# Kernel tuning notes

Measured on AMD Instinct MI355X. Metric: run time of the kernel, lower is better.

Reference implementation:

```python
import jax, jax.numpy as jnp
import numpy as np
from jax.scipy.special import logsumexp

N, K, D = 131072, 256, 32


def setup_inputs() -> dict:
    key = jax.random.key(0)
    k1, k2, k3 = jax.random.split(key, 3)
    points = jax.random.normal(k1, (N, D), dtype=jnp.float32)
    centers = jax.random.uniform(k2, (K, D), dtype=jnp.float32)
    # well-conditioned inverse-sqrt covariances (original used 15*I; scaled to
    # avoid float32 overflow in sqrt(det(covs_inv)) for D=32)
    covs_inv_sqrt = (0.5 * jnp.broadcast_to(jnp.eye(D, dtype=jnp.float32), (K, D, D))
                     + 0.02 * jax.random.normal(k3, (K, D, D), dtype=jnp.float32))
    weights = jnp.ones((K,), dtype=jnp.float32)
    threshold = jnp.zeros((1,), dtype=jnp.float32)
    return {"points": points, "centers": centers,
            "covs_inv_sqrt": covs_inv_sqrt, "weights": weights,
            "threshold": threshold}


def reference(points, centers, covs_inv_sqrt, weights, threshold):
    # refresh(): equal_clusters=True branch
    w = jnp.abs(weights)
    center_prs = w / (w.sum() + 1e-30)                       # [K]
    covs_inv = jnp.einsum('kde,kfe->kdf', covs_inv_sqrt, covs_inv_sqrt)  # [K,D,D]
    coefs = center_prs * jnp.sqrt(jnp.linalg.det(covs_inv))  # [K]

    # pairwise weighted sqdist: q_ij = (x_i - c_j)^T A_j (x_i - c_j)
    B = covs_inv.reshape(K, D * D)                           # [K, D*D]
    X2 = (points[:, :, None] * points[:, None, :]).reshape(N, D * D)  # [N, D*D]
    t_xAx = X2 @ B.T                                         # [N, K]
    m = jnp.einsum('kde,ke->kd', covs_inv, centers)          # A_j c_j, [K,D]
    t_xAc = points @ m.T                                     # [N, K]
    t_cAc = jnp.einsum('kd,kd->k', m, centers)               # [K]
    d_ij = -0.5 * (t_xAx - 2.0 * t_xAc + t_cAc[None, :])     # [N, K]

    # weighted logsumexp over centers, then subtract threshold
    ll = logsumexp(d_ij, axis=1, b=coefs[None, :])           # [N]
    return ll[:, None] - threshold[0]                        # [N, 1]
```

## Files before the change

kernel.cpp:

```cpp
#include <hip/hip_runtime.h>
#include <math.h>

#define NPTS 131072
#define KCOMP 256
#define DIM 32
#define KF 608
#define PSIF_BYTES 311296
#define WS_NEED (PSIF_BYTES + KCOMP * 4)

typedef __attribute__((ext_vector_type(8))) short short8;
typedef __attribute__((ext_vector_type(16))) float f32x16;

__device__ __forceinline__ unsigned short f2bf(float v) {
    unsigned u = __float_as_uint(v);
    u += 0x7fffu + ((u >> 16) & 1u);
    return (unsigned short)(u >> 16);
}

constexpr int L4c(int d) { return ((32 - d + 3) / 4) * 4; }
constexpr int PfxC(int d) { int s = 0; for (int i = 0; i < d; ++i) s += L4c(i); return s; }
constexpr int rowOfC(int p) { int d = 0; while (d < 31 && PfxC(d + 1) <= p) ++d; return d; }
constexpr int dOfC(int p) { return (p >= 576) ? -1 : rowOfC(p); }
constexpr int f0OfC(int p) {
    return (p >= 576) ? (p - 576) : ((rowOfC(p) & ~3) + (p - PfxC(rowOfC(p))));
}

__global__ __launch_bounds__(256) void gmm_pre(
    const float* __restrict__ S,
    const float* __restrict__ centers,
    const float* __restrict__ weights,
    unsigned short* __restrict__ PsiF,
    float* __restrict__ kc2)
{
    __shared__ float Sl[DIM][DIM + 1];
    __shared__ float As[DIM][DIM + 1];
    __shared__ float cl[DIM], ml[DIM];
    __shared__ float red[256];

    const int k = blockIdx.x, tid = threadIdx.x;

    for (int idx = tid; idx < DIM * DIM; idx += 256)
        Sl[idx >> 5][idx & 31] = S[(size_t)k * DIM * DIM + idx];
    if (tid < DIM) cl[tid] = centers[k * DIM + tid];
    __syncthreads();

    for (int idx = tid; idx < DIM * DIM; idx += 256) {
        const int d = idx >> 5, f = idx & 31;
        float a = 0.f;
#pragma unroll
        for (int e = 0; e < DIM; ++e) a = fmaf(Sl[d][e], Sl[f][e], a);
        As[d][f] = a;
    }
    __syncthreads();

    if (tid < DIM) {
        float mv = 0.f;
#pragma unroll
        for (int f = 0; f < DIM; ++f) mv = fmaf(As[tid][f], cl[f], mv);
        ml[tid] = mv;
    }
    __syncthreads();

    for (int p = tid; p < KF; p += 256) {
        float val;
        if (p < 576) {
            int d = 0, pr = 0;
            while (true) {
                const int len = ((32 - d + 3) >> 2) << 2;
                if (pr + len > p) break;
                pr += len; ++d;
            }
            const int f = (d & ~3) + (p - pr);
            val = (f < d) ? 0.f : ((f == d) ? -0.5f * As[d][d] : -As[d][f]);
        } else {
            val = ml[p - 576];
        }
        const int c = p >> 6, kk = p & 63;
        const int s = kk >> 4, qq = (kk >> 3) & 1, j = kk & 7;
        const int ct = k >> 5, ll = qq * 32 + (k & 31);
        const int g = c * 2048 + (s * 8 + ct) * 64 + ll;
        PsiF[(size_t)g * 8 + j] = f2bf(val);
    }

    red[tid] = fabsf(weights[tid]);
    __syncthreads();
    for (int off = 128; off > 0; off >>= 1) {
        if (tid < off) red[tid] += red[tid + off];
        __syncthreads();
    }
    const float wsum = red[0];

    for (int j = 0; j < DIM; ++j) {
        if (tid == 0) As[j][j] = sqrtf(As[j][j]);
        __syncthreads();
        if (tid > j && tid < DIM) As[tid][j] /= As[j][j];
        __syncthreads();
        for (int idx = tid; idx < DIM * DIM; idx += 256) {
            const int r = idx >> 5, cc = idx & 31;
            if (r > j && cc > j && cc <= r)
                As[r][cc] = fmaf(-As[r][j], As[cc][j], As[r][cc]);
        }
        __syncthreads();
    }

    if (tid == 0) {
        float ld = 0.f;
        for (int j = 0; j < DIM; ++j) ld += logf(As[j][j]);
        float cac = 0.f;
        for (int d2 = 0; d2 < DIM; ++d2) cac = fmaf(ml[d2], cl[d2], cac);
        kc2[k] = logf(fabsf(weights[k])) - logf(wsum + 1e-30f) + ld - 0.5f * cac;
    }
}

template<int P>
__device__ __forceinline__ void genQuad(const float (&x)[DIM], float* v) {
    constexpr int d = dOfC(P);
    constexpr int f0 = f0OfC(P);
#pragma unroll
    for (int j = 0; j < 4; ++j)
        v[j] = (d < 0) ? x[f0 + j] : (x[d] * x[f0 + j]);
}

template<int C, int SS>
__device__ __forceinline__ void genSite(const float (&x)[DIM], uint4* sA4,
                                        int rbg, int r32) {
    float v[8];
    genQuad<C * 64 + SS * 8>(x, v);
    genQuad<C * 64 + SS * 8 + 4>(x, v + 4);
    uint4 u;
    u.x = (unsigned)f2bf(v[0]) | ((unsigned)f2bf(v[1]) << 16);
    u.y = (unsigned)f2bf(v[2]) | ((unsigned)f2bf(v[3]) << 16);
    u.z = (unsigned)f2bf(v[4]) | ((unsigned)f2bf(v[5]) << 16);
    u.w = (unsigned)f2bf(v[6]) | ((unsigned)f2bf(v[7]) << 16);
    sA4[(SS >> 1) * 256 + rbg * 64 + (SS & 1) * 32 + r32] = u;
}

template<int C>
__device__ __forceinline__ void doChunk(const float (&x)[DIM],
    uint4* sA4, uint4* sB4, const uint4* __restrict__ PsiF4,
    f32x16 (&acc0)[4], f32x16 (&acc1)[4],
    int t, int l, int q, int rbg, int r32, int r0, int c0)
{
    constexpr int NS = (C < 9) ? 4 : 2;
    if (q == 0) {
        genSite<C, 0>(x, sA4, rbg, r32);
        genSite<C, 2>(x, sA4, rbg, r32);
        if constexpr (NS == 4) { genSite<C, 4>(x, sA4, rbg, r32); genSite<C, 6>(x, sA4, rbg, r32); }
    } else {
        genSite<C, 1>(x, sA4, rbg, r32);
        genSite<C, 3>(x, sA4, rbg, r32);
        if constexpr (NS == 4) { genSite<C, 5>(x, sA4, rbg, r32); genSite<C, 7>(x, sA4, rbg, r32); }
    }
    const uint4* src = PsiF4 + C * 2048;
#pragma unroll
    for (int m = 0; m < NS * 2; ++m)
        sB4[m * 256 + t] = src[m * 256 + t];
    __syncthreads();
#pragma unroll
    for (int s = 0; s < NS; ++s) {
        short8 a0 = __builtin_bit_cast(short8, sA4[(s * 4 + r0) * 64 + l]);
        short8 a1 = __builtin_bit_cast(short8, sA4[(s * 4 + r0 + 1) * 64 + l]);
#pragma unroll
        for (int j = 0; j < 4; ++j) {
            short8 b = __builtin_bit_cast(short8, sB4[(s * 8 + c0 + j) * 64 + l]);
            acc0[j] = __builtin_amdgcn_mfma_f32_32x32x16_bf16(a0, b, acc0[j], 0, 0, 0);
            acc1[j] = __builtin_amdgcn_mfma_f32_32x32x16_bf16(a1, b, acc1[j], 0, 0, 0);
        }
    }
    __syncthreads();
}

__device__ __forceinline__ void epiHalf(const f32x16 (&acc)[4], const float (&kcv)[4],
    int rblock, int l, int whalf, float (*sM)[2], float (*sS)[2])
{
#pragma unroll
    for (int rg = 0; rg < 16; ++rg) {
        float vals[4], m = -INFINITY;
#pragma unroll
        for (int j = 0; j < 4; ++j) { vals[j] = acc[j][rg] + kcv[j]; m = fmaxf(m, vals[j]); }
#pragma unroll
        for (int mask = 1; mask < 32; mask <<= 1) m = fmaxf(m, __shfl_xor(m, mask, 64));
        float sv = 0.f;
#pragma unroll
        for (int j = 0; j < 4; ++j) sv += __expf(vals[j] - m);
#pragma unroll
        for (int mask = 1; mask < 32; mask <<= 1) sv += __shfl_xor(sv, mask, 64);
        if ((l & 31) == 0) {
            const int R = rblock * 32 + (rg & 3) + 8 * (rg >> 2) + 4 * (l >> 5);
            sM[R][whalf] = m; sS[R][whalf] = sv;
        }
    }
}

__global__ __launch_bounds__(256, 2) void gmm_mfma(
    const float* __restrict__ points,
    const unsigned short* __restrict__ PsiF,
    const float* __restrict__ kc2,
    const float* __restrict__ thr,
    float* __restrict__ out)
{
    __shared__ uint4 sA4[1024];
    __shared__ uint4 sB4[2048];
    __shared__ float sM[128][2], sS[128][2];

    const int t = threadIdx.x;
    const int w = t >> 6, l = t & 63;
    const int row = t & 127, q = t >> 7;
    const int rbg = row >> 5, r32 = row & 31;
    const int r0 = (w >> 1) * 2, c0 = (w & 1) * 4;

    float x[DIM];
    const float4* px = (const float4*)(points + ((size_t)blockIdx.x * 128 + row) * DIM);
#pragma unroll
    for (int j2 = 0; j2 < 8; ++j2) {
        float4 v = px[j2];
        x[4 * j2 + 0] = v.x; x[4 * j2 + 1] = v.y;
        x[4 * j2 + 2] = v.z; x[4 * j2 + 3] = v.w;
    }

    f32x16 acc0[4], acc1[4];
#pragma unroll
    for (int j = 0; j < 4; ++j)
#pragma unroll
        for (int r = 0; r < 16; ++r) { acc0[j][r] = 0.f; acc1[j][r] = 0.f; }

    const uint4* PsiF4 = (const uint4*)PsiF;
    doChunk<0>(x, sA4, sB4, PsiF4, acc0, acc1, t, l, q, rbg, r32, r0, c0);
    doChunk<1>(x, sA4, sB4, PsiF4, acc0, acc1, t, l, q, rbg, r32, r0, c0);
    doChunk<2>(x, sA4, sB4, PsiF4, acc0, acc1, t, l, q, rbg, r32, r0, c0);
    doChunk<3>(x, sA4, sB4, PsiF4, acc0, acc1, t, l, q, rbg, r32, r0, c0);
    doChunk<4>(x, sA4, sB4, PsiF4, acc0, acc1, t, l, q, rbg, r32, r0, c0);
    doChunk<5>(x, sA4, sB4, PsiF4, acc0, acc1, t, l, q, rbg, r32, r0, c0);
    doChunk<6>(x, sA4, sB4, PsiF4, acc0, acc1, t, l, q, rbg, r32, r0, c0);
    doChunk<7>(x, sA4, sB4, PsiF4, acc0, acc1, t, l, q, rbg, r32, r0, c0);
    doChunk<8>(x, sA4, sB4, PsiF4, acc0, acc1, t, l, q, rbg, r32, r0, c0);
    doChunk<9>(x, sA4, sB4, PsiF4, acc0, acc1, t, l, q, rbg, r32, r0, c0);

    float kcv[4];
#pragma unroll
    for (int j = 0; j < 4; ++j) kcv[j] = kc2[(c0 + j) * 32 + (l & 31)];

    epiHalf(acc0, kcv, r0,     l, w & 1, sM, sS);
    epiHalf(acc1, kcv, r0 + 1, l, w & 1, sM, sS);
    __syncthreads();

    if (t < 128) {
        const float m0 = sM[t][0], m1 = sM[t][1];
        const float M = fmaxf(m0, m1);
        const float Sv = sS[t][0] * __expf(m0 - M) + sS[t][1] * __expf(m1 - M);
        out[(size_t)blockIdx.x * 128 + t] = M + __logf(Sv) - thr[0];
    }
}

extern "C" void kernel_launch(void* const* d_in, const int* in_sizes, int n_in,
                              void* d_out, int out_size, void* d_ws, size_t ws_size,
                              hipStream_t stream) {
    const float* points  = (const float*)d_in[0];
    const float* centers = (const float*)d_in[1];
    const float* covs    = (const float*)d_in[2];
    const float* weights = (const float*)d_in[3];
    const float* thr     = (const float*)d_in[4];
    float* out = (float*)d_out;

    unsigned short* PsiF = (unsigned short*)d_ws;
    float* kc2 = (float*)((char*)d_ws + PSIF_BYTES);

    gmm_pre<<<KCOMP, 256, 0, stream>>>(covs, centers, weights, PsiF, kc2);
    gmm_mfma<<<NPTS / 128, 256, 0, stream>>>(points, PsiF, kc2, thr, out);
}
```

Measured before the change: 161.3 us.

## Register-prefetch next PsiF chunk, cheaper bf16 packing, LU-based log-determinant

Each chunk's B tile (PsiF) is now loaded from global memory into registers one chunk ahead and then written to LDS, so global load latency overlaps with the MFMA work of the current chunk. Barrier placement is restructured to match. The bf16 packing uses a byte permute with round-half-up in place of per-element round-to-nearest-even. The precompute kernel replaces Cholesky with Gaussian elimination, taking half the log of the pivots for the log-determinant. The prefetch adds 8 uint4 registers per thread, which may pressure occupancy at 2 blocks per CU.

```diff
diff --git a/kernel.cpp b/kernel.cpp
--- a/kernel.cpp
+++ b/kernel.cpp
@@ -15,6 +15,16 @@
     unsigned u = __float_as_uint(v);
     u += 0x7fffu + ((u >> 16) & 1u);
     return (unsigned short)(u >> 16);
+}
+
+__device__ __forceinline__ unsigned pkbf(float lo, float hi) {
+#if __has_builtin(__builtin_amdgcn_perm)
+    const unsigned a = __float_as_uint(hi) + 0x8000u;
+    const unsigned b = __float_as_uint(lo) + 0x8000u;
+    return __builtin_amdgcn_perm(a, b, 0x07060302u);
+#else
+    return (unsigned)f2bf(lo) | ((unsigned)f2bf(hi) << 16);
+#endif
 }
 
 constexpr int L4c(int d) { return ((32 - d + 3) / 4) * 4; }
@@ -90,25 +100,25 @@
     }
     const float wsum = red[0];
 
-    for (int j = 0; j < DIM; ++j) {
-        if (tid == 0) As[j][j] = sqrtf(As[j][j]);
+    for (int j = 0; j < DIM - 1; ++j) {
+        const float inv = 1.0f / As[j][j];
+        for (int idx = tid; idx < DIM * DIM; idx += 256) {
+            const int r = idx >> 5, c = idx & 31;
+            if (r > j && c > j)
+                As[r][c] = fmaf(-As[r][j] * inv, As[j][c], As[r][c]);
+        }
         __syncthreads();
-        if (tid > j && tid < DIM) As[tid][j] /= As[j][j];
-        __syncthreads();
-        for (int idx = tid; idx < DIM * DIM; idx += 256) {
-            const int r = idx >> 5, cc = idx & 31;
-            if (r > j && cc > j && cc <= r)
-                As[r][cc] = fmaf(-As[r][j], As[cc][j], As[r][cc]);
-        }
-        __syncthreads();
-    }
-
+    }
+
+    if (tid < DIM) red[tid] = __logf(As[tid][tid]);
+    __syncthreads();
     if (tid == 0) {
-        float ld = 0.f;
-        for (int j = 0; j < DIM; ++j) ld += logf(As[j][j]);
+        float sl = 0.f;
+        for (int j = 0; j < DIM; ++j) sl += red[j];
         float cac = 0.f;
         for (int d2 = 0; d2 < DIM; ++d2) cac = fmaf(ml[d2], cl[d2], cac);
-        kc2[k] = logf(fabsf(weights[k])) - logf(wsum + 1e-30f) + ld - 0.5f * cac;
+        kc2[k] = __logf(fabsf(weights[k])) - __logf(wsum + 1e-30f)
+               + 0.5f * sl - 0.5f * cac;
     }
 }
 
@@ -128,20 +138,23 @@
     genQuad<C * 64 + SS * 8>(x, v);
     genQuad<C * 64 + SS * 8 + 4>(x, v + 4);
     uint4 u;
-    u.x = (unsigned)f2bf(v[0]) | ((unsigned)f2bf(v[1]) << 16);
-    u.y = (unsigned)f2bf(v[2]) | ((unsigned)f2bf(v[3]) << 16);
-    u.z = (unsigned)f2bf(v[4]) | ((unsigned)f2bf(v[5]) << 16);
-    u.w = (unsigned)f2bf(v[6]) | ((unsigned)f2bf(v[7]) << 16);
+    u.x = pkbf(v[0], v[1]);
+    u.y = pkbf(v[2], v[3]);
+    u.z = pkbf(v[4], v[5]);
+    u.w = pkbf(v[6], v[7]);
     sA4[(SS >> 1) * 256 + rbg * 64 + (SS & 1) * 32 + r32] = u;
 }
 
 template<int C>
 __device__ __forceinline__ void doChunk(const float (&x)[DIM],
     uint4* sA4, uint4* sB4, const uint4* __restrict__ PsiF4,
-    f32x16 (&acc0)[4], f32x16 (&acc1)[4],
+    f32x16 (&acc0)[4], f32x16 (&acc1)[4], uint4 (&regB)[8],
     int t, int l, int q, int rbg, int r32, int r0, int c0)
 {
-    constexpr int NS = (C < 9) ? 4 : 2;
+    constexpr int NS  = (C < 9) ? 4 : 2;
+    constexpr int NSn = (C < 8) ? 4 : ((C == 8) ? 2 : 0);
+
+    __syncthreads();
     if (q == 0) {
         genSite<C, 0>(x, sA4, rbg, r32);
         genSite<C, 2>(x, sA4, rbg, r32);
@@ -151,11 +164,16 @@
         genSite<C, 3>(x, sA4, rbg, r32);
         if constexpr (NS == 4) { genSite<C, 5>(x, sA4, rbg, r32); genSite<C, 7>(x, sA4, rbg, r32); }
     }
-    const uint4* src = PsiF4 + C * 2048;
-#pragma unroll
-    for (int m = 0; m < NS * 2; ++m)
-        sB4[m * 256 + t] = src[m * 256 + t];
-    __syncthreads();
+#pragma unroll
+    for (int m = 0; m < NS * 2; ++m) sB4[m * 256 + t] = regB[m];
+    __syncthreads();
+
+    if constexpr (NSn > 0) {
+        const uint4* srcn = PsiF4 + (C + 1) * 2048;
+#pragma unroll
+        for (int m = 0; m < NSn * 2; ++m) regB[m] = srcn[m * 256 + t];
+    }
+
 #pragma unroll
     for (int s = 0; s < NS; ++s) {
         short8 a0 = __builtin_bit_cast(short8, sA4[(s * 4 + r0) * 64 + l]);
@@ -167,7 +185,6 @@
             acc1[j] = __builtin_amdgcn_mfma_f32_32x32x16_bf16(a1, b, acc1[j], 0, 0, 0);
         }
     }
-    __syncthreads();
 }
 
 __device__ __forceinline__ void epiHalf(const f32x16 (&acc)[4], const float (&kcv)[4],
@@ -209,6 +226,11 @@
     const int rbg = row >> 5, r32 = row & 31;
     const int r0 = (w >> 1) * 2, c0 = (w & 1) * 4;
 
+    const uint4* PsiF4 = (const uint4*)PsiF;
+    uint4 regB[8];
+#pragma unroll
+    for (int m = 0; m < 8; ++m) regB[m] = PsiF4[m * 256 + t];
+
     float x[DIM];
     const float4* px = (const float4*)(points + ((size_t)blockIdx.x * 128 + row) * DIM);
 #pragma unroll
@@ -224,17 +246,16 @@
 #pragma unroll
         for (int r = 0; r < 16; ++r) { acc0[j][r] = 0.f; acc1[j][r] = 0.f; }
 
-    const uint4* PsiF4 = (const uint4*)PsiF;
-    doChunk<0>(x, sA4, sB4, PsiF4, acc0, acc1, t, l, q, rbg, r32, r0, c0);
-    doChunk<1>(x, sA4, sB4, PsiF4, acc0, acc1, t, l, q, rbg, r32, r0, c0);
-    doChunk<2>(x, sA4, sB4, PsiF4, acc0, acc1, t, l, q, rbg, r32, r0, c0);
-    doChunk<3>(x, sA4, sB4, PsiF4, acc0, acc1, t, l, q, rbg, r32, r0, c0);
-    doChunk<4>(x, sA4, sB4, PsiF4, acc0, acc1, t, l, q, rbg, r32, r0, c0);
-    doChunk<5>(x, sA4, sB4, PsiF4, acc0, acc1, t, l, q, rbg, r32, r0, c0);
-    doChunk<6>(x, sA4, sB4, PsiF4, acc0, acc1, t, l, q, rbg, r32, r0, c0);
-    doChunk<7>(x, sA4, sB4, PsiF4, acc0, acc1, t, l, q, rbg, r32, r0, c0);
-    doChunk<8>(x, sA4, sB4, PsiF4, acc0, acc1, t, l, q, rbg, r32, r0, c0);
-    doChunk<9>(x, sA4, sB4, PsiF4, acc0, acc1, t, l, q, rbg, r32, r0, c0);
+    doChunk<0>(x, sA4, sB4, PsiF4, acc0, acc1, regB, t, l, q, rbg, r32, r0, c0);
+    doChunk<1>(x, sA4, sB4, PsiF4, acc0, acc1, regB, t, l, q, rbg, r32, r0, c0);
+    doChunk<2>(x, sA4, sB4, PsiF4, acc0, acc1, regB, t, l, q, rbg, r32, r0, c0);
+    doChunk<3>(x, sA4, sB4, PsiF4, acc0, acc1, regB, t, l, q, rbg, r32, r0, c0);
+    doChunk<4>(x, sA4, sB4, PsiF4, acc0, acc1, regB, t, l, q, rbg, r32, r0, c0);
+    doChunk<5>(x, sA4, sB4, PsiF4, acc0, acc1, regB, t, l, q, rbg, r32, r0, c0);
+    doChunk<6>(x, sA4, sB4, PsiF4, acc0, acc1, regB, t, l, q, rbg, r32, r0, c0);
+    doChunk<7>(x, sA4, sB4, PsiF4, acc0, acc1, regB, t, l, q, rbg, r32, r0, c0);
+    doChunk<8>(x, sA4, sB4, PsiF4, acc0, acc1, regB, t, l, q, rbg, r32, r0, c0);
+    doChunk<9>(x, sA4, sB4, PsiF4, acc0, acc1, regB, t, l, q, rbg, r32, r0, c0);
 
     float kcv[4];
 #pragma unroll
```

Result: slower. 200.1 us (+24.0%).
